# Optimization experiments

Hardware: AMD Instinct MI355X
Metric: run time of the kernel (lower is better)

Reference implementation:

```python
import jax, jax.numpy as jnp
import numpy as np

T, B, E, H, V = 50, 64, 1024, 1024, 32000
NL = 2


def setup_inputs() -> dict:
    key = jax.random.key(0)
    ks = jax.random.split(key, 16)
    def rn(k, shape, fan_in):
        return jax.random.normal(k, shape, jnp.float32) * (1.0 / np.sqrt(fan_in))
    return {
        "word": jax.random.randint(ks[0], (B,), 0, V),
        "seq": jax.random.randint(ks[1], (T, B), 0, V),
        "emb": jax.random.normal(ks[2], (V, E), jnp.float32) * 0.05,
        "w2h_W": rn(ks[3], (H, E), E),
        "w2h_b": jnp.zeros((H,), jnp.float32),
        "W_ih0": rn(ks[4], (4 * H, 2 * E), 2 * E),
        "W_hh0": rn(ks[5], (4 * H, H), H),
        "b_ih0": jnp.zeros((4 * H,), jnp.float32),
        "b_hh0": jnp.zeros((4 * H,), jnp.float32),
        "W_ih1": rn(ks[6], (4 * H, H), H),
        "W_hh1": rn(ks[7], (4 * H, H), H),
        "b_ih1": jnp.zeros((4 * H,), jnp.float32),
        "b_hh1": jnp.zeros((4 * H,), jnp.float32),
        "dec_W": rn(ks[8], (V, H), H),
        "dec_b": jnp.zeros((V,), jnp.float32),
    }


def _lstm_layer(x, Wih, Whh, bih, bhh, h0, c0):
    """x: [T,B,D] -> hs: [T,B,H]. PyTorch gate order: i,f,g,o."""
    b = bih + bhh
    # precompute input contribution for all timesteps (one big GEMM)
    xg = jnp.einsum('tbd,gd->tbg', x, Wih) + b  # [T,B,4H]

    def step(carry, xt):
        h, c = carry
        gates = xt + h @ Whh.T
        i, f, g, o = jnp.split(gates, 4, axis=-1)
        c = jax.nn.sigmoid(f) * c + jax.nn.sigmoid(i) * jnp.tanh(g)
        h = jax.nn.sigmoid(o) * jnp.tanh(c)
        return (h, c), h

    (hT, cT), hs = jax.lax.scan(step, (h0, c0), xg)
    return hs, hT, cT


def reference(word, seq, emb, w2h_W, w2h_b, W_ih0, W_hh0, b_ih0, b_hh0,
              W_ih1, W_hh1, b_ih1, b_hh1, dec_W, dec_b):
    word_emb = emb[word]            # [B,E]
    seq_emb = emb[seq]              # [T,B,E]
    # init_hidden: c = word2hidden(word_emb) expanded over layers, h = zeros
    c0 = word_emb @ w2h_W.T + w2h_b          # [B,H]
    h0 = jnp.zeros_like(c0)
    # use_input: concat word_emb to every timestep input
    x0 = jnp.concatenate(
        [jnp.broadcast_to(word_emb[None], (T, B, E)), seq_emb], axis=-1)  # [T,B,2E]
    hs0, h0T, c0T = _lstm_layer(x0, W_ih0, W_hh0, b_ih0, b_hh0, h0, c0)
    hs1, h1T, c1T = _lstm_layer(hs0, W_ih1, W_hh1, b_ih1, b_hh1, h0, c0)
    outputs = hs1.reshape(T * B, H)
    decoded = outputs @ dec_W.T + dec_b      # [T*B, V]
    h_final = jnp.stack([h0T, h1T], 0)       # [NL,B,H]
    c_final = jnp.stack([c0T, c1T], 0)
    return decoded, h_final, c_final
```

## Files before the change

### kernel.cpp

```cpp
#include <hip/hip_runtime.h>
#include <cstddef>


static constexpr int T_ = 50, B_ = 64, E_ = 1024, H_ = 1024, V_ = 32000;
static constexpr int G_ = 4096;

typedef unsigned short u16;
typedef unsigned int u32;
typedef unsigned long long u64;
typedef __attribute__((ext_vector_type(8))) short bf16x8;
typedef __attribute__((ext_vector_type(8))) unsigned short u16x8;
typedef __attribute__((ext_vector_type(4))) float f32x4;

__device__ __forceinline__ int perm_g(int n) {
  return ((n >> 4) & 3) * H_ + (n >> 6) * 16 + (n & 15);
}
__device__ __forceinline__ u16 bf16_rn(float x) {
  union { float f; unsigned u; } a; a.f = x;
  unsigned r = a.u + 0x7fffu + ((a.u >> 16) & 1u);
  return (u16)(r >> 16);
}
__device__ __forceinline__ float bf16_f(u16 h) {
  union { float f; unsigned u; } a; a.u = ((unsigned)h) << 16;
  return a.f;
}
__device__ __forceinline__ float sigm(float x) { return 1.f / (1.f + __expf(-x)); }

__global__ void fill_zero(float* p, int n) {
  int i = blockIdx.x * blockDim.x + threadIdx.x;
  if (i < n) p[i] = 0.f;
}
__global__ void bias_perm(const float* a, const float* b, float* dst) {
  int n = blockIdx.x * 256 + threadIdx.x;
  int s = perm_g(n);
  dst[n] = a[s] + b[s];
}

__global__ void conv_w(const float* __restrict__ src, int srcld, int coloff,
                       const int* __restrict__ gidx, int PERM, int rows,
                       u16* __restrict__ dst) {
  int idx = blockIdx.x * 256 + threadIdx.x;
  int r = idx >> 7, kc = (idx & 127) << 3;
  if (r >= rows) return;
  int s = gidx ? gidx[r] : (PERM ? perm_g(r) : r);
  const float* p = src + (size_t)s * srcld + coloff + kc;
  float4 v0 = *(const float4*)p, v1 = *(const float4*)(p + 4);
  float vv[8] = {v0.x, v0.y, v0.z, v0.w, v1.x, v1.y, v1.z, v1.w};
  u16 hi[8], lo[8];
#pragma unroll
  for (int i = 0; i < 8; ++i) {
    hi[i] = bf16_rn(vv[i]);
    lo[i] = bf16_rn(vv[i] - bf16_f(hi[i]));
  }
  u16x8 c0, c1;
#pragma unroll
  for (int i = 0; i < 4; ++i) {
    c0[2 * i] = hi[i];     c0[2 * i + 1] = lo[i];
    c1[2 * i] = hi[4 + i]; c1[2 * i + 1] = lo[4 + i];
  }
  int seg = kc >> 5;
  int ch0 = (kc >> 2) & 7;
  size_t base = (size_t)r * 2048 + seg * 64;
  *(u16x8*)&dst[base + (size_t)((ch0 ^ (r & 7)) << 3)] = c0;
  *(u16x8*)&dst[base + (size_t)(((ch0 | 1) ^ (r & 7)) << 3)] = c1;
}

template<int BM, int BN, int BK, int TM, int TN>
__launch_bounds__(256)
__global__ void gemm_nt(
    const float* __restrict__ A, const int* __restrict__ Aidx, int lda,
    const float* __restrict__ W, int ldw, int koff,
    const float* __restrict__ bias, float* __restrict__ C, int ldc,
    int M, int N, int K) {
  constexpr int TX = BN / TN;
  constexpr int TY = BM / TM;
  static_assert(TX * TY == 256, "thread geometry");
  __shared__ float As[BK][BM + 4];
  __shared__ float Ws[BK][BN + 4];
  const int tid = threadIdx.x;
  const int tx = tid % TX, ty = tid / TX;
  const int m0 = blockIdx.y * BM, n0 = blockIdx.x * BN;
  float acc[TM][TN];
#pragma unroll
  for (int i = 0; i < TM; ++i)
#pragma unroll
    for (int j = 0; j < TN; ++j) acc[i][j] = 0.f;
  constexpr int AV = (BM * BK) / 4;
  constexpr int WV = (BN * BK) / 4;
  constexpr int KV = BK / 4;
  for (int k0 = 0; k0 < K; k0 += BK) {
#pragma unroll
    for (int lp = 0; lp < (AV + 255) / 256; ++lp) {
      int e = tid + lp * 256;
      if (e < AV) {
        int r = e / KV, kq = e % KV;
        int m = m0 + r;
        float4 v = make_float4(0.f, 0.f, 0.f, 0.f);
        if (m < M) {
          int row = Aidx ? Aidx[m] : m;
          v = *(const float4*)&A[(size_t)row * lda + k0 + kq * 4];
        }
        As[kq * 4 + 0][r] = v.x; As[kq * 4 + 1][r] = v.y;
        As[kq * 4 + 2][r] = v.z; As[kq * 4 + 3][r] = v.w;
      }
    }
#pragma unroll
    for (int lp = 0; lp < (WV + 255) / 256; ++lp) {
      int e = tid + lp * 256;
      if (e < WV) {
        int cc = e / KV, kq = e % KV;
        int n = n0 + cc;
        float4 v = make_float4(0.f, 0.f, 0.f, 0.f);
        if (n < N)
          v = *(const float4*)&W[(size_t)n * ldw + koff + k0 + kq * 4];
        Ws[kq * 4 + 0][cc] = v.x; Ws[kq * 4 + 1][cc] = v.y;
        Ws[kq * 4 + 2][cc] = v.z; Ws[kq * 4 + 3][cc] = v.w;
      }
    }
    __syncthreads();
#pragma unroll
    for (int kk = 0; kk < BK; ++kk) {
      float a[TM], b[TN];
#pragma unroll
      for (int i = 0; i < TM; ++i) a[i] = As[kk][ty * TM + i];
#pragma unroll
      for (int j = 0; j < TN; ++j) b[j] = Ws[kk][tx * TN + j];
#pragma unroll
      for (int i = 0; i < TM; ++i)
#pragma unroll
        for (int j = 0; j < TN; ++j)
          acc[i][j] += a[i] * b[j];
    }
    __syncthreads();
  }
#pragma unroll
  for (int i = 0; i < TM; ++i) {
    int m = m0 + ty * TM + i;
    if (m >= M) continue;
#pragma unroll
    for (int j = 0; j < TN; ++j) {
      int n = n0 + tx * TN + j;
      if (n >= N) continue;
      float v = acc[i][j];
      if (bias) v += bias[n];
      C[(size_t)m * ldc + n] = v;
    }
  }
}

__launch_bounds__(256)
__global__ void gemm_bt(const u16* __restrict__ A, int Mrows,
                        const u16* __restrict__ Wb,
                        const float* __restrict__ bias,
                        const float* __restrict__ Dadd, int ldd, int dmask,
                        float* __restrict__ C, int ldc, int N, int nbx,
                        int mt, int ord) {
  __shared__ u16 lsA[128 * 64];
  __shared__ u16 lsB[128 * 64];

  int nwg = gridDim.x, bid = blockIdx.x;
  int q = nwg >> 3, r = nwg & 7;
  int xcd = bid & 7, base = bid >> 3;
  int wg = (xcd < r ? xcd * (q + 1) : r * (q + 1) + (xcd - r) * q) + base;
  int bx, by;
  if (ord) { by = wg % mt; bx = wg / mt; } else { bx = wg % nbx; by = wg / nbx; }
  const int m0 = by * 128, n0 = bx * 128;

  const int tid = threadIdx.x, w = tid >> 6, l = tid & 63;
  const int lr = l & 15, lq = l >> 4;
  const int wm = (w >> 1) * 64, wn = (w & 1) * 64;

  f32x4 acc[4][4] = {};

  for (int kt = 0; kt < 32; ++kt) {
#pragma unroll
    for (int i = 0; i < 4; ++i) {
      int rb = w * 32 + i * 8;
      int gm = m0 + rb + (l >> 3);
      if (gm > Mrows - 1) gm = Mrows - 1;
      const u16* ga = A + (size_t)gm * 2048 + kt * 64 + (l & 7) * 8;
      __builtin_amdgcn_global_load_lds(
          (const __attribute__((address_space(1))) void*)ga,
          (__attribute__((address_space(3))) void*)(lsA + rb * 64), 16, 0, 0);
      const u16* gb = Wb + (size_t)(n0 + rb + (l >> 3)) * 2048 + kt * 64 + (l & 7) * 8;
      __builtin_amdgcn_global_load_lds(
          (const __attribute__((address_space(1))) void*)gb,
          (__attribute__((address_space(3))) void*)(lsB + rb * 64), 16, 0, 0);
    }
    asm volatile("s_waitcnt vmcnt(0)" ::: "memory");
    __syncthreads();

    bf16x8 af[4][2], bfr[4][2];
#pragma unroll
    for (int i = 0; i < 4; ++i) {
      int ar = wm + i * 16 + lr;
#pragma unroll
      for (int s = 0; s < 2; ++s)
        af[i][s] = *(const bf16x8*)&lsA[ar * 64 + (((s << 2) + lq) ^ (ar & 7)) * 8];
    }
#pragma unroll
    for (int j = 0; j < 4; ++j) {
      int br = wn + j * 16 + lr;
#pragma unroll
      for (int s = 0; s < 2; ++s)
        bfr[j][s] = *(const bf16x8*)&lsB[br * 64 + (((s << 2) + lq) ^ (br & 7)) * 8];
    }
#pragma unroll
    for (int i = 0; i < 4; ++i)
#pragma unroll
      for (int j = 0; j < 4; ++j) {
        acc[i][j] = __builtin_amdgcn_mfma_f32_16x16x32_bf16(af[i][0], bfr[j][0], acc[i][j], 0, 0, 0);
        acc[i][j] = __builtin_amdgcn_mfma_f32_16x16x32_bf16(af[i][1], bfr[j][1], acc[i][j], 0, 0, 0);
      }
    __syncthreads();
  }

#pragma unroll
  for (int i = 0; i < 4; ++i) {
    int mbase = m0 + wm + i * 16 + lq * 4;
#pragma unroll
    for (int j = 0; j < 4; ++j) {
      int n = n0 + wn + j * 16 + lr;
      float badd = bias ? bias[n] : 0.f;
#pragma unroll
      for (int rr = 0; rr < 4; ++rr) {
        int m = mbase + rr;
        if (m >= Mrows) continue;
        float v = acc[i][j][rr] + badd;
        if (Dadd) {
          int dr = (dmask < 0) ? m : (m & dmask);
          v += Dadd[(size_t)dr * ldd + n];
        }
        C[(size_t)m * ldc + n] = v;
      }
    }
  }
}

__launch_bounds__(256)
__global__ void gemm_sp(
    const float* __restrict__ A, int lda,
    const float* __restrict__ W, int ldw,
    const float* __restrict__ bias,
    float* __restrict__ C, int ldc, int M, int N, int K, int nbx) {
  __shared__ u16 As_h[128][40], As_l[128][40];
  __shared__ u16 Ws_h[128][40], Ws_l[128][40];
  int nwg = gridDim.x, bid = blockIdx.x;
  int q = nwg >> 3, r = nwg & 7;
  int xcd = bid & 7, base = bid >> 3;
  int wg = (xcd < r ? xcd * (q + 1) : r * (q + 1) + (xcd - r) * q) + base;
  int bx = wg % nbx, by = wg / nbx;
  const int m0 = by * 128, n0 = bx * 128;
  const int tid = threadIdx.x;
  const int wave = tid >> 6, lane = tid & 63;
  const int lr = lane & 15, lq = lane >> 4;
  const int wm = (wave >> 1) * 64, wn = (wave & 1) * 64;
  f32x4 acc[4][4] = {};
  for (int k0 = 0; k0 < K; k0 += 32) {
#pragma unroll
    for (int lp = 0; lp < 4; ++lp) {
      int s = tid + lp * 256;
      int row = s >> 3, kq = s & 7;
      float4 v = make_float4(0.f, 0.f, 0.f, 0.f);
      int gm = m0 + row;
      if (gm < M)
        v = *(const float4*)&A[(size_t)gm * lda + k0 + kq * 4];
      u16 h0 = bf16_rn(v.x), h1 = bf16_rn(v.y), h2 = bf16_rn(v.z), h3 = bf16_rn(v.w);
      u16 l0 = bf16_rn(v.x - bf16_f(h0)), l1 = bf16_rn(v.y - bf16_f(h1));
      u16 l2 = bf16_rn(v.z - bf16_f(h2)), l3 = bf16_rn(v.w - bf16_f(h3));
      *(uint2*)&As_h[row][kq * 4] =
          make_uint2((u32)h0 | ((u32)h1 << 16), (u32)h2 | ((u32)h3 << 16));
      *(uint2*)&As_l[row][kq * 4] =
          make_uint2((u32)l0 | ((u32)l1 << 16), (u32)l2 | ((u32)l3 << 16));
    }
#pragma unroll
    for (int lp = 0; lp < 4; ++lp) {
      int s = tid + lp * 256;
      int col = s >> 3, kq = s & 7;
      int n = n0 + col;
      float4 v = make_float4(0.f, 0.f, 0.f, 0.f);
      if (n < N)
        v = *(const float4*)&W[(size_t)n * ldw + k0 + kq * 4];
      u16 h0 = bf16_rn(v.x), h1 = bf16_rn(v.y), h2 = bf16_rn(v.z), h3 = bf16_rn(v.w);
      u16 l0 = bf16_rn(v.x - bf16_f(h0)), l1 = bf16_rn(v.y - bf16_f(h1));
      u16 l2 = bf16_rn(v.z - bf16_f(h2)), l3 = bf16_rn(v.w - bf16_f(h3));
      *(uint2*)&Ws_h[col][kq * 4] =
          make_uint2((u32)h0 | ((u32)h1 << 16), (u32)h2 | ((u32)h3 << 16));
      *(uint2*)&Ws_l[col][kq * 4] =
          make_uint2((u32)l0 | ((u32)l1 << 16), (u32)l2 | ((u32)l3 << 16));
    }
    __syncthreads();
    bf16x8 ah[4], al[4], bh[4], bl[4];
#pragma unroll
    for (int i = 0; i < 4; ++i) {
      ah[i] = *(const bf16x8*)&As_h[wm + i * 16 + lr][lq * 8];
      al[i] = *(const bf16x8*)&As_l[wm + i * 16 + lr][lq * 8];
    }
#pragma unroll
    for (int j = 0; j < 4; ++j) {
      bh[j] = *(const bf16x8*)&Ws_h[wn + j * 16 + lr][lq * 8];
      bl[j] = *(const bf16x8*)&Ws_l[wn + j * 16 + lr][lq * 8];
    }
#pragma unroll
    for (int i = 0; i < 4; ++i)
#pragma unroll
      for (int j = 0; j < 4; ++j) {
        acc[i][j] = __builtin_amdgcn_mfma_f32_16x16x32_bf16(ah[i], bh[j], acc[i][j], 0, 0, 0);
        acc[i][j] = __builtin_amdgcn_mfma_f32_16x16x32_bf16(ah[i], bl[j], acc[i][j], 0, 0, 0);
        acc[i][j] = __builtin_amdgcn_mfma_f32_16x16x32_bf16(al[i], bh[j], acc[i][j], 0, 0, 0);
      }
    __syncthreads();
  }
#pragma unroll
  for (int i = 0; i < 4; ++i) {
    int mbase = m0 + wm + i * 16 + lq * 4;
#pragma unroll
    for (int j = 0; j < 4; ++j) {
      int n = n0 + wn + j * 16 + lr;
      if (n >= N) continue;
      float badd = bias ? bias[n] : 0.f;
#pragma unroll
      for (int rr = 0; rr < 4; ++rr) {
        int m = mbase + rr;
        if (m >= M) continue;
        C[(size_t)m * ldc + n] = acc[i][j][rr] + badd;
      }
    }
  }
}

__device__ __forceinline__ void gemm_half(
    const u32* __restrict__ hp, int rg, int w, int lr, int lq,
    const bf16x8 (&bfr)[8][4], f32x4 (&acc)[2][4]) {
  bf16x8 af[8][2];
#pragma unroll
  for (int s = 0; s < 8; ++s)
#pragma unroll
    for (int mt = 0; mt < 2; ++mt) {
      int m = rg * 32 + mt * 16 + lr;
      int seg = w * 4 + (s >> 1);
      int cis = ((((s & 1) << 2) + lq) ^ (lr & 7));
      const u32* p = hp + (size_t)m * 1024 + seg * 32 + cis * 4;
      asm volatile("global_load_dwordx4 %0, %1, off sc0 sc1"
                   : "=v"(af[s][mt]) : "v"(p) : "memory");
    }
  asm volatile("s_waitcnt vmcnt(0)" ::: "memory");
  __builtin_amdgcn_sched_barrier(0);
#pragma unroll
  for (int s = 0; s < 8; ++s)
#pragma unroll
    for (int mt = 0; mt < 2; ++mt)
#pragma unroll
      for (int nt = 0; nt < 4; ++nt)
        acc[mt][nt] = __builtin_amdgcn_mfma_f32_16x16x32_bf16(
            af[s][mt], bfr[s][nt], acc[mt][nt], 0, 0, 0);
}

__device__ __forceinline__ void poll_flags(const u32* flags, int rg, int l, u32 tgt) {
  int guard = 0;
  for (;;) {
    u32 v = __hip_atomic_load(flags + (size_t)((rg << 6) + l) * 4,
                              __ATOMIC_RELAXED, __HIP_MEMORY_SCOPE_AGENT);
    if (__all(v >= tgt)) break;
    if (++guard > (1 << 23)) break;
    __builtin_amdgcn_s_sleep(1);
  }
}

template<bool DUAL, bool EMIT>
__launch_bounds__(512, 1)
__global__ void rnn_dual(const u16* __restrict__ Whh0b, const u16* __restrict__ Whh1b,
                         const u16* __restrict__ Wih1b,
                         const float* __restrict__ xg0all, const float* __restrict__ bias1p,
                         float* __restrict__ cL0, float* __restrict__ hL0,
                         float* __restrict__ cL1, float* __restrict__ hL1,
                         u32* __restrict__ h0s, u32* __restrict__ h1s,
                         float* __restrict__ hsf,
                         u32* __restrict__ flg0, u32* __restrict__ flg1, int T) {
  __shared__ float partial[8][32][68];

  const int bid = blockIdx.x;
  const int x = bid & 7, j = bid >> 3;
  const int layer = DUAL ? (j & 1) : 0;
  const int idx = DUAL ? (j >> 1) : j;
  const int ct = x * 8 + (idx & 7);
  const int rg = idx >> 3;
  const int tid = threadIdx.x, w = tid >> 6, l = tid & 63;
  const int lr = l & 15, lq = l >> 4;

  const u16* WbA = (layer ? Whh1b : Whh0b) + (size_t)(ct * 64) * 2048;
  bf16x8 bfragA[8][4];
#pragma unroll
  for (int s = 0; s < 8; ++s)
#pragma unroll
    for (int nt = 0; nt < 4; ++nt) {
      int row = nt * 16 + lr;
      int seg = w * 4 + (s >> 1);
      int cis = ((((s & 1) << 2) + lq) ^ (lr & 7));
      bfragA[s][nt] = *(const bf16x8*)&WbA[(size_t)row * 2048 + seg * 64 + cis * 8];
    }
  bf16x8 bfragX[8][4];
  if (DUAL && layer) {
    const u16* WbX = Wih1b + (size_t)(ct * 64) * 2048;
#pragma unroll
    for (int s = 0; s < 8; ++s)
#pragma unroll
      for (int nt = 0; nt < 4; ++nt) {
        int row = nt * 16 + lr;
        int seg = w * 4 + (s >> 1);
        int cis = ((((s & 1) << 2) + lq) ^ (lr & 7));
        bfragX[s][nt] = *(const bf16x8*)&WbX[(size_t)row * 2048 + seg * 64 + cis * 8];
      }
  }

  const int cm = tid >> 4, cu = tid & 15;
  const int m_c = rg * 32 + cm;
  const int unit = ct * 16 + cu;
  float* cL = layer ? cL1 : cL0;
  float* hL = layer ? hL1 : hL0;
  u32* hsl = layer ? h1s : h0s;
  u32* flgS = layer ? flg1 : flg0;
  float creg = cL[m_c * H_ + unit];
  float bset[4];
  if (layer) {
#pragma unroll
    for (int g = 0; g < 4; ++g)
      bset[g] = bias1p[ct * 64 + g * 16 + cu];
  }

  for (int t = 0; t < T; ++t) {
    float xgv[4];
    if (!layer) {
      const float* xg = xg0all + (size_t)t * ((size_t)B_ * G_);
#pragma unroll
      for (int g = 0; g < 4; ++g)
        xgv[g] = xg[(size_t)m_c * G_ + ct * 64 + g * 16 + cu];
    } else {
#pragma unroll
      for (int g = 0; g < 4; ++g) xgv[g] = bset[g];
    }

    f32x4 acc[2][4] = {};

    if (layer) {
      if (t && w == 0) poll_flags(flg1, rg, l, (u32)t);
      __syncthreads();
      gemm_half(h1s + (size_t)t * (B_ * 1024), rg, w, lr, lq, bfragA, acc);
      if (w == 0) poll_flags(flg0, rg, l, (u32)(t + 1));
      __syncthreads();
      gemm_half(h0s + (size_t)(t + 1) * (B_ * 1024), rg, w, lr, lq, bfragX, acc);
    } else {
      if (t && w == 0) poll_flags(flg0, rg, l, (u32)t);
      __syncthreads();
      gemm_half(h0s + (size_t)t * (B_ * 1024), rg, w, lr, lq, bfragA, acc);
    }

#pragma unroll
    for (int mt = 0; mt < 2; ++mt)
#pragma unroll
      for (int nt = 0; nt < 4; ++nt)
#pragma unroll
        for (int rr = 0; rr < 4; ++rr)
          partial[w][mt * 16 + lq * 4 + rr][nt * 16 + lr] = acc[mt][nt][rr];
    __syncthreads();

    float g4[4];
#pragma unroll
    for (int g = 0; g < 4; ++g) {
      float ssum = xgv[g];
#pragma unroll
      for (int p = 0; p < 8; ++p) ssum += partial[p][cm][g * 16 + cu];
      g4[g] = ssum;
    }
    float cn = sigm(g4[1]) * creg + sigm(g4[0]) * tanhf(g4[2]);
    float hn = sigm(g4[3]) * tanhf(cn);
    creg = cn;
    if (EMIT && layer) hsf[(size_t)t * (B_ * H_) + m_c * H_ + unit] = hn;
    if (t == T - 1) { cL[m_c * H_ + unit] = cn; hL[m_c * H_ + unit] = hn; }
    u16 hh = bf16_rn(hn);
    u16 hl2 = bf16_rn(hn - bf16_f(hh));
    u32 packed = (u32)hh | ((u32)hl2 << 16);
    u32* hnext = hsl + (size_t)(t + 1) * (B_ * 1024);
    u32 hidx = m_c * 1024 + ((unit >> 5) << 5) +
               ((((unit >> 2) & 7) ^ (m_c & 7)) << 2) + (unit & 3);
    {
      u32* sp = hnext + hidx;
      asm volatile("global_store_dword %0, %1, off sc0 sc1"
                   :: "v"(sp), "v"(packed) : "memory");
    }

    if (!layer || t < T - 1) {
      asm volatile("s_waitcnt vmcnt(0)" ::: "memory");
      __syncthreads();
      if (tid == 0)
        __hip_atomic_store(flgS + (size_t)((rg << 6) + ct) * 4, (u32)(t + 1),
                           __ATOMIC_RELAXED, __HIP_MEMORY_SCOPE_AGENT);
    }
  }
}

__launch_bounds__(256)
__global__ void rnn_step(const u16* __restrict__ hprev, const u16* __restrict__ Wb,
                         const float* __restrict__ xg,
                         float* __restrict__ c, float* __restrict__ hf,
                         u32* __restrict__ hout) {
  __shared__ char smem[32768];
  u16* lsA = (u16*)smem;
  u16* lsB = (u16*)(smem + 16384);
  const int nt = blockIdx.x, n0 = nt * 64;
  const int tid = threadIdx.x, w = tid >> 6, l = tid & 63;
  const int lr = l & 15, lq = l >> 4;
  f32x4 acc[4] = {};
  for (int kt = 0; kt < 16; ++kt) {
#pragma unroll
    for (int i = 0; i < 4; ++i) {
      int rb = w * 16 + i * 4;
      const u16* ga = hprev + (size_t)(rb + (l >> 4)) * 2048 + kt * 128 + (l & 15) * 8;
      __builtin_amdgcn_global_load_lds(
          (const __attribute__((address_space(1))) void*)ga,
          (__attribute__((address_space(3))) void*)(lsA + rb * 128), 16, 0, 0);
      const u16* gb = Wb + (size_t)(n0 + rb + (l >> 4)) * 2048 + kt * 128 + (l & 15) * 8;
      __builtin_amdgcn_global_load_lds(
          (const __attribute__((address_space(1))) void*)gb,
          (__attribute__((address_space(3))) void*)(lsB + rb * 128), 16, 0, 0);
    }
    asm volatile("s_waitcnt vmcnt(0)" ::: "memory");
    __syncthreads();
    bf16x8 af[4];
    int ar = w * 16 + lr;
#pragma unroll
    for (int s = 0; s < 4; ++s)
      af[s] = *(const bf16x8*)&lsA[ar * 128 + (s >> 1) * 64 + ((((s & 1) << 2) + lq) ^ (ar & 7)) * 8];
#pragma unroll
    for (int j = 0; j < 4; ++j) {
      int br = j * 16 + lr;
#pragma unroll
      for (int s = 0; s < 4; ++s) {
        bf16x8 bv = *(const bf16x8*)&lsB[br * 128 + (s >> 1) * 64 + ((((s & 1) << 2) + lq) ^ (br & 7)) * 8];
        acc[j] = __builtin_amdgcn_mfma_f32_16x16x32_bf16(af[s], bv, acc[j], 0, 0, 0);
      }
    }
    __syncthreads();
  }
  float* gsh = (float*)smem;
#pragma unroll
  for (int j = 0; j < 4; ++j)
#pragma unroll
    for (int rr = 0; rr < 4; ++rr)
      gsh[(w * 16 + lq * 4 + rr) * 68 + j * 16 + lr] = acc[j][rr];
  __syncthreads();
  const int ui = tid & 15, mq = tid >> 4;
#pragma unroll
  for (int mr = 0; mr < 4; ++mr) {
    int m = mr * 16 + mq;
    float gi = gsh[m * 68 + 0 + ui]  + xg[(size_t)m * G_ + n0 + 0 + ui];
    float gf = gsh[m * 68 + 16 + ui] + xg[(size_t)m * G_ + n0 + 16 + ui];
    float gg = gsh[m * 68 + 32 + ui] + xg[(size_t)m * G_ + n0 + 32 + ui];
    float go = gsh[m * 68 + 48 + ui] + xg[(size_t)m * G_ + n0 + 48 + ui];
    int unit = nt * 16 + ui;
    int ci = m * H_ + unit;
    float cn = sigm(gf) * c[ci] + sigm(gi) * tanhf(gg);
    float hn = sigm(go) * tanhf(cn);
    c[ci] = cn;
    hf[ci] = hn;
    u16 hh = bf16_rn(hn);
    u16 hl = bf16_rn(hn - bf16_f(hh));
    u32 hidx = m * 1024 + ((unit >> 5) << 5) +
               ((((unit >> 2) & 7) ^ (m & 7)) << 2) + (unit & 3);
    hout[hidx] = (u32)hh | ((u32)hl << 16);
  }
}

extern "C" void kernel_launch(void* const* d_in, const int* in_sizes, int n_in,
                              void* d_out, int out_size, void* d_ws, size_t ws_size,
                              hipStream_t stream) {
  const int*   word  = (const int*)  d_in[0];
  const int*   seq   = (const int*)  d_in[1];
  const float* emb   = (const float*)d_in[2];
  const float* w2h_W = (const float*)d_in[3];
  const float* w2h_b = (const float*)d_in[4];
  const float* W_ih0 = (const float*)d_in[5];
  const float* W_hh0 = (const float*)d_in[6];
  const float* b_ih0 = (const float*)d_in[7];
  const float* b_hh0 = (const float*)d_in[8];
  const float* W_ih1 = (const float*)d_in[9];
  const float* W_hh1 = (const float*)d_in[10];
  const float* b_ih1 = (const float*)d_in[11];
  const float* b_hh1 = (const float*)d_in[12];
  const float* dec_W = (const float*)d_in[13];
  const float* dec_b = (const float*)d_in[14];

  float* out = (float*)d_out;
  float* hL0 = out + 102400000;
  float* hL1 = hL0 + B_ * H_;
  float* cL0 = out + 102531072;
  float* cL1 = cL0 + B_ * H_;

  float* xg0      = out;
  u16*   x0w_bf   = (u16*)(out + 13200000);
  u16*   x0seq_bf = (u16*)(out + 13300000);
  u32*   hs0slots = (u32*)(out + 16600000);
  u16*   wih0a_bf = (u16*)(out + 20000000);
  u16*   wih0b_bf = (u16*)(out + 24200000);
  u16*   wih1_bf  = (u16*)(out + 28400000);
  u16*   whh0_bf  = (u16*)(out + 32600000);
  u16*   whh1_bf  = (u16*)(out + 36800000);
  float* y_w      = out + 73800000;
  float* bias0p   = out + 74400000;
  float* bias1p   = out + 74410000;
  float* xg1      = out + 87560192;
  u32*   h1alt    = (u32*)(out + 91000000);
  u32*   flg0     = (u32*)(out + 101000000);
  u32*   flg1     = (u32*)(out + 101004096);
  u32*   hbfA     = (u32*)(out + 101100000);
  u32*   hbfB     = (u32*)(out + 101200000);

  const size_t need_hs1  = (size_t)T_ * B_ * H_ * 4;
  const size_t need_full = (size_t)V_ * 2048 * 2 + (size_t)(T_ + 1) * B_ * 1024 * 4;
  const bool tier1 = ws_size >= need_full;
  const bool tier2 = !tier1 && ws_size >= need_hs1;

  u16*   decW_bf  = (u16*)d_ws;
  u32*   hs1slots = (u32*)d_ws + (size_t)V_ * 1024;
  float* hs1f     = (float*)d_ws;

  fill_zero<<<32, 256, 0, stream>>>(out + 101000000, 8192);
  fill_zero<<<256, 256, 0, stream>>>((float*)hs0slots, 65536);
  if (tier1) fill_zero<<<256, 256, 0, stream>>>((float*)hs1slots, 65536);
  else if (tier2) fill_zero<<<256, 256, 0, stream>>>((float*)h1alt, 65536);
  bias_perm<<<16, 256, 0, stream>>>(b_ih0, b_hh0, bias0p);
  bias_perm<<<16, 256, 0, stream>>>(b_ih1, b_hh1, bias1p);

  gemm_nt<64, 64, 16, 4, 4><<<dim3(16, 1), 256, 0, stream>>>(
      emb, word, E_, w2h_W, E_, 0, w2h_b, cL0, H_, B_, H_, E_);
  gemm_nt<64, 64, 16, 4, 4><<<dim3(16, 1), 256, 0, stream>>>(
      emb, word, E_, w2h_W, E_, 0, w2h_b, cL1, H_, B_, H_, E_);

  conv_w<<<2048, 256, 0, stream>>>(W_ih0, 2 * E_, 0,  nullptr, 1, G_, wih0a_bf);
  conv_w<<<2048, 256, 0, stream>>>(W_ih0, 2 * E_, E_, nullptr, 1, G_, wih0b_bf);
  conv_w<<<2048, 256, 0, stream>>>(W_ih1, H_, 0, nullptr, 1, G_, wih1_bf);
  conv_w<<<2048, 256, 0, stream>>>(W_hh0, H_, 0, nullptr, 1, G_, whh0_bf);
  conv_w<<<2048, 256, 0, stream>>>(W_hh1, H_, 0, nullptr, 1, G_, whh1_bf);
  conv_w<<<32,   256, 0, stream>>>(emb, E_, 0, word, 0, B_, x0w_bf);
  conv_w<<<1600, 256, 0, stream>>>(emb, E_, 0, seq, 0, T_ * B_, x0seq_bf);
  if (tier1)
    conv_w<<<16000, 256, 0, stream>>>(dec_W, H_, 0, nullptr, 0, V_, decW_bf);

  gemm_bt<<<32, 256, 0, stream>>>(x0w_bf, B_, wih0a_bf, bias0p,
                                  nullptr, 0, -1, y_w, G_, G_, 32, 1, 0);
  gemm_bt<<<800, 256, 0, stream>>>(x0seq_bf, T_ * B_, wih0b_bf, nullptr,
                                   y_w, G_, 63, xg0, G_, G_, 32, 25, 0);

  if (tier1) {
    rnn_dual<true, false><<<256, 512, 0, stream>>>(
        whh0_bf, whh1_bf, wih1_bf, xg0, bias1p,
        cL0, hL0, cL1, hL1, hs0slots, hs1slots, nullptr, flg0, flg1, T_);
    gemm_bt<<<6250, 256, 0, stream>>>((const u16*)(hs1slots + (size_t)B_ * 1024),
                                      T_ * B_, decW_bf, dec_b,
                                      nullptr, 0, -1, out, V_, V_, 250, 25, 1);
  } else if (tier2) {
    rnn_dual<true, true><<<256, 512, 0, stream>>>(
        whh0_bf, whh1_bf, wih1_bf, xg0, bias1p,
        cL0, hL0, cL1, hL1, hs0slots, h1alt, hs1f, flg0, flg1, T_);
    gemm_sp<<<6250, 256, 0, stream>>>(
        hs1f, H_, dec_W, H_, dec_b, out, V_, T_ * B_, V_, H_, 250);
  } else {
    rnn_dual<false, false><<<128, 512, 0, stream>>>(
        whh0_bf, whh1_bf, wih1_bf, xg0, bias1p,
        cL0, hL0, cL1, hL1, hs0slots, nullptr, nullptr, flg0, flg1, T_);
    gemm_bt<<<800, 256, 0, stream>>>((const u16*)(hs0slots + (size_t)B_ * 1024),
                                     T_ * B_, wih1_bf, bias1p,
                                     nullptr, 0, -1, xg1, G_, G_, 32, 25, 0);
    for (int t = 0; t < T_; ++t) {
      const u16* hp = t ? (const u16*)((t & 1) ? hbfA : hbfB) : (const u16*)hs0slots;
      u32* ho = (t & 1) ? hbfB : hbfA;
      rnn_step<<<64, 256, 0, stream>>>(
          hp, whh1_bf, xg1 + (size_t)t * B_ * G_, cL1, hL1, ho);
      gemm_sp<<<250, 256, 0, stream>>>(
          hL1, H_, dec_W, H_, dec_b, out + (size_t)t * B_ * V_, V_, B_, V_, H_, 250);
    }
  }
}
```

Measured before the change: 1.851 ms.

## Fuse decoder GEMM into persistent LSTM kernel, overlapping chunks with recurrence

Adds a decode_chunk routine inside the persistent rnn_dual kernel. Every 4 timesteps, each of the first 250 blocks waits on the layer-1 flags and computes 256 rows of the vocab projection. It converts fp32 dec_W to split bf16 hi/lo on the fly instead of running a separate conversion pass and a trailing decoder GEMM. A new workspace tier holds h states, xg0 and the converted recurrent weights. The aim is to hide the large decoder GEMM behind the latency-bound recurrence, at the cost of extra LDS (96KB), extra barriers that may stall the recurrence critical path, and repeated dec_W conversion per chunk.

Result: slower. 2.520 ms (+36.2%).

```diff
diff --git a/kernel.cpp b/kernel.cpp
--- a/kernel.cpp
+++ b/kernel.cpp
@@ -367,7 +367,88 @@
   }
 }
 
-template<bool DUAL, bool EMIT>
+__device__ __forceinline__ void decode_chunk(
+    char* smem, int ch, int nMt, int n0,
+    const u32* __restrict__ h1s, const float* __restrict__ decW,
+    const float* __restrict__ dec_b, float* __restrict__ outC,
+    int tid, int w, int lr, int lq) {
+  u16* As = (u16*)smem;
+  u16* Bs = (u16*)(smem + 65536);
+  const int nrows = nMt * 64;
+  f32x4 acc[4][4] = {};
+
+  for (int kc = 0; kc < 16; ++kc) {
+    __syncthreads();
+#pragma unroll
+    for (int i = 0; i < 8; ++i) {
+      int e = tid + i * 512;
+      int row = e >> 4, part = e & 15;
+      if (row < nrows) {
+        const u32* src = h1s + (size_t)(4 * ch + 1 + (row >> 6)) * (B_ * 1024)
+                       + (size_t)(row & 63) * 1024 + kc * 64 + part * 4;
+        uint4 v = *(const uint4*)src;
+        *(uint4*)&As[row * 128 + part * 8] = v;
+      }
+    }
+#pragma unroll
+    for (int i = 0; i < 2; ++i) {
+      int e = tid + i * 512;
+      int row = e >> 3, kc8 = e & 7;
+      const float* p = decW + (size_t)(n0 + row) * 1024 + kc * 64 + kc8 * 8;
+      float4 v0 = *(const float4*)p, v1 = *(const float4*)(p + 4);
+      float vv[8] = {v0.x, v0.y, v0.z, v0.w, v1.x, v1.y, v1.z, v1.w};
+      u16 hi[8], lo[8];
+#pragma unroll
+      for (int q2 = 0; q2 < 8; ++q2) {
+        hi[q2] = bf16_rn(vv[q2]);
+        lo[q2] = bf16_rn(vv[q2] - bf16_f(hi[q2]));
+      }
+      u16x8 c0, c1;
+#pragma unroll
+      for (int q2 = 0; q2 < 4; ++q2) {
+        c0[2 * q2] = hi[q2];     c0[2 * q2 + 1] = lo[q2];
+        c1[2 * q2] = hi[4 + q2]; c1[2 * q2 + 1] = lo[4 + q2];
+      }
+      int segl = kc8 >> 2;
+      int ch0 = (kc8 & 3) * 2;
+      u16* dst = Bs + row * 128 + segl * 64;
+      *(u16x8*)&dst[(ch0 ^ (row & 7)) << 3] = c0;
+      *(u16x8*)&dst[((ch0 | 1) ^ (row & 7)) << 3] = c1;
+    }
+    __syncthreads();
+#pragma unroll
+    for (int ks = 0; ks < 4; ++ks) {
+      int segl = ks >> 1;
+      int cgrp = (ks & 1) << 2;
+      int cis = (cgrp + lq) ^ (lr & 7);
+      bf16x8 bfr = *(const bf16x8*)&Bs[(w * 16 + lr) * 128 + segl * 64 + cis * 8];
+#pragma unroll
+      for (int mt = 0; mt < 4; ++mt)
+#pragma unroll
+        for (int mf = 0; mf < 4; ++mf) {
+          int row = mt * 64 + mf * 16 + lr;
+          bf16x8 af = *(const bf16x8*)&As[row * 128 + segl * 64 + cis * 8];
+          acc[mt][mf] = __builtin_amdgcn_mfma_f32_16x16x32_bf16(af, bfr, acc[mt][mf], 0, 0, 0);
+        }
+    }
+  }
+  __syncthreads();
+  int col = n0 + w * 16 + lr;
+  float badd = dec_b[col];
+#pragma unroll
+  for (int mt = 0; mt < 4; ++mt) {
+    if (mt >= nMt) break;
+#pragma unroll
+    for (int mf = 0; mf < 4; ++mf)
+#pragma unroll
+      for (int rr = 0; rr < 4; ++rr) {
+        int mrow = ch * 256 + mt * 64 + mf * 16 + lq * 4 + rr;
+        outC[(size_t)mrow * V_ + col] = acc[mt][mf][rr] + badd;
+      }
+  }
+}
+
+template<bool DUAL, bool EMIT, bool DEC>
 __launch_bounds__(512, 1)
 __global__ void rnn_dual(const u16* __restrict__ Whh0b, const u16* __restrict__ Whh1b,
                          const u16* __restrict__ Wih1b,
@@ -376,8 +457,11 @@
                          float* __restrict__ cL1, float* __restrict__ hL1,
                          u32* __restrict__ h0s, u32* __restrict__ h1s,
                          float* __restrict__ hsf,
-                         u32* __restrict__ flg0, u32* __restrict__ flg1, int T) {
-  __shared__ float partial[8][32][68];
+                         u32* __restrict__ flg0, u32* __restrict__ flg1,
+                         const float* __restrict__ decW, const float* __restrict__ dec_b,
+                         float* __restrict__ outC, int T) {
+  __shared__ char smem[98304];
+  float* partial = (float*)smem;
 
   const int bid = blockIdx.x;
   const int x = bid & 7, j = bid >> 3;
@@ -461,7 +545,7 @@
       for (int nt = 0; nt < 4; ++nt)
 #pragma unroll
         for (int rr = 0; rr < 4; ++rr)
-          partial[w][mt * 16 + lq * 4 + rr][nt * 16 + lr] = acc[mt][nt][rr];
+          partial[(w * 32 + mt * 16 + lq * 4 + rr) * 68 + nt * 16 + lr] = acc[mt][nt][rr];
     __syncthreads();
 
     float g4[4];
@@ -469,7 +553,7 @@
     for (int g = 0; g < 4; ++g) {
       float ssum = xgv[g];
 #pragma unroll
-      for (int p = 0; p < 8; ++p) ssum += partial[p][cm][g * 16 + cu];
+      for (int p = 0; p < 8; ++p) ssum += partial[(p * 32 + cm) * 68 + g * 16 + cu];
       g4[g] = ssum;
     }
     float cn = sigm(g4[1]) * creg + sigm(g4[0]) * tanhf(g4[2]);
@@ -489,13 +573,30 @@
                    :: "v"(sp), "v"(packed) : "memory");
     }
 
-    if (!layer || t < T - 1) {
-      asm volatile("s_waitcnt vmcnt(0)" ::: "memory");
-      __syncthreads();
-      if (tid == 0)
-        __hip_atomic_store(flgS + (size_t)((rg << 6) + ct) * 4, (u32)(t + 1),
-                           __ATOMIC_RELAXED, __HIP_MEMORY_SCOPE_AGENT);
-    }
+    asm volatile("s_waitcnt vmcnt(0)" ::: "memory");
+    __syncthreads();
+    if (tid == 0)
+      __hip_atomic_store(flgS + (size_t)((rg << 6) + ct) * 4, (u32)(t + 1),
+                         __ATOMIC_RELAXED, __HIP_MEMORY_SCOPE_AGENT);
+
+    if (DEC) {
+      if (t >= 5 && ((t - 5) & 3) == 0) {
+        int ch = (t - 5) >> 2;
+        u32 tgt = (u32)(4 * ch + 4);
+        if (w == 0) { poll_flags(flg1, 0, l, tgt); poll_flags(flg1, 1, l, tgt); }
+        __syncthreads();
+        if (bid < 250)
+          decode_chunk(smem, ch, 4, bid * 128, h1s, decW, dec_b, outC, tid, w, lr, lq);
+        __syncthreads();
+      }
+    }
+  }
+
+  if (DEC) {
+    if (w == 0) { poll_flags(flg1, 0, l, (u32)T); poll_flags(flg1, 1, l, (u32)T); }
+    __syncthreads();
+    if (bid < 250)
+      decode_chunk(smem, 12, 2, bid * 128, h1s, decW, dec_b, outC, tid, w, lr, lq);
   }
 }
 
@@ -532,22 +633,22 @@
     for (int s = 0; s < 4; ++s)
       af[s] = *(const bf16x8*)&lsA[ar * 128 + (s >> 1) * 64 + ((((s & 1) << 2) + lq) ^ (ar & 7)) * 8];
 #pragma unroll
-    for (int j = 0; j < 4; ++j) {
-      int br = j * 16 + lr;
+    for (int jj = 0; jj < 4; ++jj) {
+      int br = jj * 16 + lr;
 #pragma unroll
       for (int s = 0; s < 4; ++s) {
         bf16x8 bv = *(const bf16x8*)&lsB[br * 128 + (s >> 1) * 64 + ((((s & 1) << 2) + lq) ^ (br & 7)) * 8];
-        acc[j] = __builtin_amdgcn_mfma_f32_16x16x32_bf16(af[s], bv, acc[j], 0, 0, 0);
+        acc[jj] = __builtin_amdgcn_mfma_f32_16x16x32_bf16(af[s], bv, acc[jj], 0, 0, 0);
       }
     }
     __syncthreads();
   }
   float* gsh = (float*)smem;
 #pragma unroll
-  for (int j = 0; j < 4; ++j)
+  for (int jj = 0; jj < 4; ++jj)
 #pragma unroll
     for (int rr = 0; rr < 4; ++rr)
-      gsh[(w * 16 + lq * 4 + rr) * 68 + j * 16 + lr] = acc[j][rr];
+      gsh[(w * 16 + lq * 4 + rr) * 68 + jj * 16 + lr] = acc[jj][rr];
   __syncthreads();
   const int ui = tid & 15, mq = tid >> 4;
 #pragma unroll
@@ -596,88 +697,120 @@
   float* cL0 = out + 102531072;
   float* cL1 = cL0 + B_ * H_;
 
-  float* xg0      = out;
   u16*   x0w_bf   = (u16*)(out + 13200000);
   u16*   x0seq_bf = (u16*)(out + 13300000);
-  u32*   hs0slots = (u32*)(out + 16600000);
   u16*   wih0a_bf = (u16*)(out + 20000000);
   u16*   wih0b_bf = (u16*)(out + 24200000);
-  u16*   wih1_bf  = (u16*)(out + 28400000);
-  u16*   whh0_bf  = (u16*)(out + 32600000);
-  u16*   whh1_bf  = (u16*)(out + 36800000);
   float* y_w      = out + 73800000;
   float* bias0p   = out + 74400000;
-  float* bias1p   = out + 74410000;
-  float* xg1      = out + 87560192;
-  u32*   h1alt    = (u32*)(out + 91000000);
-  u32*   flg0     = (u32*)(out + 101000000);
-  u32*   flg1     = (u32*)(out + 101004096);
-  u32*   hbfA     = (u32*)(out + 101100000);
-  u32*   hbfB     = (u32*)(out + 101200000);
-
-  const size_t need_hs1  = (size_t)T_ * B_ * H_ * 4;
-  const size_t need_full = (size_t)V_ * 2048 * 2 + (size_t)(T_ + 1) * B_ * 1024 * 4;
-  const bool tier1 = ws_size >= need_full;
-  const bool tier2 = !tier1 && ws_size >= need_hs1;
-
-  u16*   decW_bf  = (u16*)d_ws;
-  u32*   hs1slots = (u32*)d_ws + (size_t)V_ * 1024;
-  float* hs1f     = (float*)d_ws;
-
-  fill_zero<<<32, 256, 0, stream>>>(out + 101000000, 8192);
-  fill_zero<<<256, 256, 0, stream>>>((float*)hs0slots, 65536);
-  if (tier1) fill_zero<<<256, 256, 0, stream>>>((float*)hs1slots, 65536);
-  else if (tier2) fill_zero<<<256, 256, 0, stream>>>((float*)h1alt, 65536);
-  bias_perm<<<16, 256, 0, stream>>>(b_ih0, b_hh0, bias0p);
-  bias_perm<<<16, 256, 0, stream>>>(b_ih1, b_hh1, bias1p);
-
-  gemm_nt<64, 64, 16, 4, 4><<<dim3(16, 1), 256, 0, stream>>>(
-      emb, word, E_, w2h_W, E_, 0, w2h_b, cL0, H_, B_, H_, E_);
-  gemm_nt<64, 64, 16, 4, 4><<<dim3(16, 1), 256, 0, stream>>>(
-      emb, word, E_, w2h_W, E_, 0, w2h_b, cL1, H_, B_, H_, E_);
-
-  conv_w<<<2048, 256, 0, stream>>>(W_ih0, 2 * E_, 0,  nullptr, 1, G_, wih0a_bf);
-  conv_w<<<2048, 256, 0, stream>>>(W_ih0, 2 * E_, E_, nullptr, 1, G_, wih0b_bf);
-  conv_w<<<2048, 256, 0, stream>>>(W_ih1, H_, 0, nullptr, 1, G_, wih1_bf);
-  conv_w<<<2048, 256, 0, stream>>>(W_hh0, H_, 0, nullptr, 1, G_, whh0_bf);
-  conv_w<<<2048, 256, 0, stream>>>(W_hh1, H_, 0, nullptr, 1, G_, whh1_bf);
-  conv_w<<<32,   256, 0, stream>>>(emb, E_, 0, word, 0, B_, x0w_bf);
-  conv_w<<<1600, 256, 0, stream>>>(emb, E_, 0, seq, 0, T_ * B_, x0seq_bf);
-  if (tier1)
-    conv_w<<<16000, 256, 0, stream>>>(dec_W, H_, 0, nullptr, 0, V_, decW_bf);
-
-  gemm_bt<<<32, 256, 0, stream>>>(x0w_bf, B_, wih0a_bf, bias0p,
-                                  nullptr, 0, -1, y_w, G_, G_, 32, 1, 0);
-  gemm_bt<<<800, 256, 0, stream>>>(x0seq_bf, T_ * B_, wih0b_bf, nullptr,
-                                   y_w, G_, 63, xg0, G_, G_, 32, 25, 0);
-
-  if (tier1) {
-    rnn_dual<true, false><<<256, 512, 0, stream>>>(
-        whh0_bf, whh1_bf, wih1_bf, xg0, bias1p,
-        cL0, hL0, cL1, hL1, hs0slots, hs1slots, nullptr, flg0, flg1, T_);
-    gemm_bt<<<6250, 256, 0, stream>>>((const u16*)(hs1slots + (size_t)B_ * 1024),
-                                      T_ * B_, decW_bf, dec_b,
-                                      nullptr, 0, -1, out, V_, V_, 250, 25, 1);
-  } else if (tier2) {
-    rnn_dual<true, true><<<256, 512, 0, stream>>>(
-        whh0_bf, whh1_bf, wih1_bf, xg0, bias1p,
-        cL0, hL0, cL1, hL1, hs0slots, h1alt, hs1f, flg0, flg1, T_);
-    gemm_sp<<<6250, 256, 0, stream>>>(
-        hs1f, H_, dec_W, H_, dec_b, out, V_, T_ * B_, V_, H_, 250);
+
+  const size_t need0    = 129600000;
+  const size_t need_hs1 = (size_t)T_ * B_ * H_ * 4;
+  const bool tier0 = ws_size >= need0;
+  const bool tier2 = !tier0 && ws_size >= need_hs1;
+
+  if (tier0) {
+    char* wsb = (char*)d_ws;
+    u32*   h1p    = (u32*)wsb;
+    u32*   h0p    = (u32*)(wsb + 13369344);
+    float* xg0p   = (float*)(wsb + 26738688);
+    u16*   whh0p  = (u16*)(wsb + 79167488);
+    u16*   whh1p  = (u16*)(wsb + 95944704);
+    u16*   wih1p  = (u16*)(wsb + 112721920);
+    float* b1p    = (float*)(wsb + 129499136);
+    u32*   f0p    = (u32*)(wsb + 129515520);
+    u32*   f1p    = (u32*)(wsb + 129519616);
+
+    fill_zero<<<8, 256, 0, stream>>>((float*)f0p, 2048);
+    fill_zero<<<256, 256, 0, stream>>>((float*)h0p, 65536);
+    fill_zero<<<256, 256, 0, stream>>>((float*)h1p, 65536);
+    bias_perm<<<16, 256, 0, stream>>>(b_ih0, b_hh0, bias0p);
+    bias_perm<<<16, 256, 0, stream>>>(b_ih1, b_hh1, b1p);
+
+    gemm_nt<64, 64, 16, 4, 4><<<dim3(16, 1), 256, 0, stream>>>(
+        emb, word, E_, w2h_W, E_, 0, w2h_b, cL0, H_, B_, H_, E_);
+    gemm_nt<64, 64, 16, 4, 4><<<dim3(16, 1), 256, 0, stream>>>(
+        emb, word, E_, w2h_W, E_, 0, w2h_b, cL1, H_, B_, H_, E_);
+
+    conv_w<<<2048, 256, 0, stream>>>(W_ih0, 2 * E_, 0,  nullptr, 1, G_, wih0a_bf);
+    conv_w<<<2048, 256, 0, stream>>>(W_ih0, 2 * E_, E_, nullptr, 1, G_, wih0b_bf);
+    conv_w<<<2048, 256, 0, stream>>>(W_ih1, H_, 0, nullptr, 1, G_, wih1p);
+    conv_w<<<2048, 256, 0, stream>>>(W_hh0, H_, 0, nullptr, 1, G_, whh0p);
+    conv_w<<<2048, 256, 0, stream>>>(W_hh1, H_, 0, nullptr, 1, G_, whh1p);
+    conv_w<<<32,   256, 0, stream>>>(emb, E_, 0, word, 0, B_, x0w_bf);
+    conv_w<<<1600, 256, 0, stream>>>(emb, E_, 0, seq, 0, T_ * B_, x0seq_bf);
+
+    gemm_bt<<<32, 256, 0, stream>>>(x0w_bf, B_, wih0a_bf, bias0p,
+                                    nullptr, 0, -1, y_w, G_, G_, 32, 1, 0);
+    gemm_bt<<<800, 256, 0, stream>>>(x0seq_bf, T_ * B_, wih0b_bf, nullptr,
+                                     y_w, G_, 63, xg0p, G_, G_, 32, 25, 0);
+
+    rnn_dual<true, false, true><<<256, 512, 0, stream>>>(
+        whh0p, whh1p, wih1p, xg0p, b1p,
+        cL0, hL0, cL1, hL1, h0p, h1p, nullptr, f0p, f1p,
+        dec_W, dec_b, out, T_);
   } else {
-    rnn_dual<false, false><<<128, 512, 0, stream>>>(
-        whh0_bf, whh1_bf, wih1_bf, xg0, bias1p,
-        cL0, hL0, cL1, hL1, hs0slots, nullptr, nullptr, flg0, flg1, T_);
-    gemm_bt<<<800, 256, 0, stream>>>((const u16*)(hs0slots + (size_t)B_ * 1024),
-                                     T_ * B_, wih1_bf, bias1p,
-                                     nullptr, 0, -1, xg1, G_, G_, 32, 25, 0);
-    for (int t = 0; t < T_; ++t) {
-      const u16* hp = t ? (const u16*)((t & 1) ? hbfA : hbfB) : (const u16*)hs0slots;
-      u32* ho = (t & 1) ? hbfB : hbfA;
-      rnn_step<<<64, 256, 0, stream>>>(
-          hp, whh1_bf, xg1 + (size_t)t * B_ * G_, cL1, hL1, ho);
-      gemm_sp<<<250, 256, 0, stream>>>(
-          hL1, H_, dec_W, H_, dec_b, out + (size_t)t * B_ * V_, V_, B_, V_, H_, 250);
-    }
-  }
-}
+    float* xg0      = out;
+    u32*   hs0slots = (u32*)(out + 16600000);
+    u16*   wih1_bf  = (u16*)(out + 28400000);
+    u16*   whh0_bf  = (u16*)(out + 32600000);
+    u16*   whh1_bf  = (u16*)(out + 36800000);
+    float* bias1p   = out + 74410000;
+    float* xg1      = out + 87560192;
+    u32*   h1alt    = (u32*)(out + 91000000);
+    u32*   flg0     = (u32*)(out + 101000000);
+    u32*   flg1     = (u32*)(out + 101004096);
+    u32*   hbfA     = (u32*)(out + 101100000);
+    u32*   hbfB     = (u32*)(out + 101200000);
+    float* hs1f     = (float*)d_ws;
+
+    fill_zero<<<32, 256, 0, stream>>>(out + 101000000, 8192);
+    fill_zero<<<256, 256, 0, stream>>>((float*)hs0slots, 65536);
+    if (tier2) fill_zero<<<256, 256, 0, stream>>>((float*)h1alt, 65536);
+    bias_perm<<<16, 256, 0, stream>>>(b_ih0, b_hh0, bias0p);
+    bias_perm<<<16, 256, 0, stream>>>(b_ih1, b_hh1, bias1p);
+
+    gemm_nt<64, 64, 16, 4, 4><<<dim3(16, 1), 256, 0, stream>>>(
+        emb, word, E_, w2h_W, E_, 0, w2h_b, cL0, H_, B_, H_, E_);
+    gemm_nt<64, 64, 16, 4, 4><<<dim3(16, 1), 256, 0, stream>>>(
+        emb, word, E_, w2h_W, E_, 0, w2h_b, cL1, H_, B_, H_, E_);
+
+    conv_w<<<2048, 256, 0, stream>>>(W_ih0, 2 * E_, 0,  nullptr, 1, G_, wih0a_bf);
+    conv_w<<<2048, 256, 0, stream>>>(W_ih0, 2 * E_, E_, nullptr, 1, G_, wih0b_bf);
+    conv_w<<<2048, 256, 0, stream>>>(W_ih1, H_, 0, nullptr, 1, G_, wih1_bf);
+    conv_w<<<2048, 256, 0, stream>>>(W_hh0, H_, 0, nullptr, 1, G_, whh0_bf);
+    conv_w<<<2048, 256, 0, stream>>>(W_hh1, H_, 0, nullptr, 1, G_, whh1_bf);
+    conv_w<<<32,   256, 0, stream>>>(emb, E_, 0, word, 0, B_, x0w_bf);
+    conv_w<<<1600, 256, 0, stream>>>(emb, E_, 0, seq, 0, T_ * B_, x0seq_bf);
+
+    gemm_bt<<<32, 256, 0, stream>>>(x0w_bf, B_, wih0a_bf, bias0p,
+                                    nullptr, 0, -1, y_w, G_, G_, 32, 1, 0);
+    gemm_bt<<<800, 256, 0, stream>>>(x0seq_bf, T_ * B_, wih0b_bf, nullptr,
+                                     y_w, G_, 63, xg0, G_, G_, 32, 25, 0);
+
+    if (tier2) {
+      rnn_dual<true, true, false><<<256, 512, 0, stream>>>(
+          whh0_bf, whh1_bf, wih1_bf, xg0, bias1p,
+          cL0, hL0, cL1, hL1, hs0slots, h1alt, hs1f, flg0, flg1,
+          nullptr, nullptr, nullptr, T_);
+      gemm_sp<<<6250, 256, 0, stream>>>(
+          hs1f, H_, dec_W, H_, dec_b, out, V_, T_ * B_, V_, H_, 250);
+    } else {
+      rnn_dual<false, false, false><<<128, 512, 0, stream>>>(
+          whh0_bf, whh1_bf, wih1_bf, xg0, bias1p,
+          cL0, hL0, cL1, hL1, hs0slots, nullptr, nullptr, flg0, flg1,
+          nullptr, nullptr, nullptr, T_);
+      gemm_bt<<<800, 256, 0, stream>>>((const u16*)(hs0slots + (size_t)B_ * 1024),
+                                       T_ * B_, wih1_bf, bias1p,
+                                       nullptr, 0, -1, xg1, G_, G_, 32, 25, 0);
+      for (int t = 0; t < T_; ++t) {
+        const u16* hp = t ? (const u16*)((t & 1) ? hbfA : hbfB) : (const u16*)hs0slots;
+        u32* ho = (t & 1) ? hbfB : hbfA;
+        rnn_step<<<64, 256, 0, stream>>>(
+            hp, whh1_bf, xg1 + (size_t)t * B_ * G_, cL1, hL1, ho);
+        gemm_sp<<<250, 256, 0, stream>>>(
+            hL1, H_, dec_W, H_, dec_b, out + (size_t)t * B_ * V_, V_, B_, V_, H_, 250);
+      }
+    }
+  }
+}
```

## Double-buffer gemm_bt LDS loads and let each wave poll its own source flags

Applied to the files above, without the earlier changes.

The main bf16 GEMM now uses two LDS buffers and issues the global-to-LDS loads for the next k-tile before computing on the current one. It waits with a partial vmcnt so memory latency overlaps the MFMA work. In the recurrent kernel, each wave now polls only the 8 producer flags it depends on, replacing one wave polling all flags followed by a block-wide barrier. This removes a __syncthreads per GEMM half, at the cost of doubled LDS use in gemm_bt and a finer-grained dependency check that must cover every row each wave reads.

After: 2.006 ms. 1.08x slower.

```diff
diff --git a/kernel.cpp b/kernel.cpp
--- a/kernel.cpp
+++ b/kernel.cpp
@@ -155,8 +155,8 @@
                         const float* __restrict__ Dadd, int ldd, int dmask,
                         float* __restrict__ C, int ldc, int N, int nbx,
                         int mt, int ord) {
-  __shared__ u16 lsA[128 * 64];
-  __shared__ u16 lsB[128 * 64];
+  __shared__ u16 lsA[2][128 * 64];
+  __shared__ u16 lsB[2][128 * 64];
 
   int nwg = gridDim.x, bid = blockIdx.x;
   int q = nwg >> 3, r = nwg & 7;
@@ -172,22 +172,33 @@
 
   f32x4 acc[4][4] = {};
 
+#define GBT_STAGE(KT, BUF)                                                     \
+  {                                                                            \
+    _Pragma("unroll")                                                          \
+    for (int i_ = 0; i_ < 4; ++i_) {                                           \
+      int rb_ = w * 32 + i_ * 8;                                               \
+      int gm_ = m0 + rb_ + (l >> 3);                                           \
+      if (gm_ > Mrows - 1) gm_ = Mrows - 1;                                    \
+      const u16* ga_ = A + (size_t)gm_ * 2048 + (KT) * 64 + (l & 7) * 8;       \
+      __builtin_amdgcn_global_load_lds(                                        \
+          (const __attribute__((address_space(1))) void*)ga_,                  \
+          (__attribute__((address_space(3))) void*)(lsA[BUF] + rb_ * 64), 16, 0, 0); \
+      const u16* gb_ = Wb + (size_t)(n0 + rb_ + (l >> 3)) * 2048 + (KT) * 64 + (l & 7) * 8; \
+      __builtin_amdgcn_global_load_lds(                                        \
+          (const __attribute__((address_space(1))) void*)gb_,                  \
+          (__attribute__((address_space(3))) void*)(lsB[BUF] + rb_ * 64), 16, 0, 0); \
+    }                                                                          \
+  }
+
+  GBT_STAGE(0, 0)
   for (int kt = 0; kt < 32; ++kt) {
-#pragma unroll
-    for (int i = 0; i < 4; ++i) {
-      int rb = w * 32 + i * 8;
-      int gm = m0 + rb + (l >> 3);
-      if (gm > Mrows - 1) gm = Mrows - 1;
-      const u16* ga = A + (size_t)gm * 2048 + kt * 64 + (l & 7) * 8;
-      __builtin_amdgcn_global_load_lds(
-          (const __attribute__((address_space(1))) void*)ga,
-          (__attribute__((address_space(3))) void*)(lsA + rb * 64), 16, 0, 0);
-      const u16* gb = Wb + (size_t)(n0 + rb + (l >> 3)) * 2048 + kt * 64 + (l & 7) * 8;
-      __builtin_amdgcn_global_load_lds(
-          (const __attribute__((address_space(1))) void*)gb,
-          (__attribute__((address_space(3))) void*)(lsB + rb * 64), 16, 0, 0);
-    }
-    asm volatile("s_waitcnt vmcnt(0)" ::: "memory");
+    const int cur = kt & 1;
+    if (kt < 31) {
+      GBT_STAGE(kt + 1, cur ^ 1)
+      asm volatile("s_waitcnt vmcnt(8)" ::: "memory");
+    } else {
+      asm volatile("s_waitcnt vmcnt(0)" ::: "memory");
+    }
     __syncthreads();
 
     bf16x8 af[4][2], bfr[4][2];
@@ -196,14 +207,14 @@
       int ar = wm + i * 16 + lr;
 #pragma unroll
       for (int s = 0; s < 2; ++s)
-        af[i][s] = *(const bf16x8*)&lsA[ar * 64 + (((s << 2) + lq) ^ (ar & 7)) * 8];
+        af[i][s] = *(const bf16x8*)&lsA[cur][ar * 64 + (((s << 2) + lq) ^ (ar & 7)) * 8];
     }
 #pragma unroll
     for (int j = 0; j < 4; ++j) {
       int br = wn + j * 16 + lr;
 #pragma unroll
       for (int s = 0; s < 2; ++s)
-        bfr[j][s] = *(const bf16x8*)&lsB[br * 64 + (((s << 2) + lq) ^ (br & 7)) * 8];
+        bfr[j][s] = *(const bf16x8*)&lsB[cur][br * 64 + (((s << 2) + lq) ^ (br & 7)) * 8];
     }
 #pragma unroll
     for (int i = 0; i < 4; ++i)
@@ -214,6 +225,7 @@
       }
     __syncthreads();
   }
+#undef GBT_STAGE
 
 #pragma unroll
   for (int i = 0; i < 4; ++i) {
@@ -356,11 +368,13 @@
             af[s][mt], bfr[s][nt], acc[mt][nt], 0, 0, 0);
 }
 
-__device__ __forceinline__ void poll_flags(const u32* flags, int rg, int l, u32 tgt) {
+__device__ __forceinline__ void poll_src(const u32* flags, int rg, int w, int l, u32 tgt) {
   int guard = 0;
   for (;;) {
-    u32 v = __hip_atomic_load(flags + (size_t)((rg << 6) + l) * 4,
-                              __ATOMIC_RELAXED, __HIP_MEMORY_SCOPE_AGENT);
+    u32 v = tgt;
+    if (l < 8)
+      v = __hip_atomic_load(flags + (size_t)((rg << 6) + (w << 3) + l) * 4,
+                            __ATOMIC_RELAXED, __HIP_MEMORY_SCOPE_AGENT);
     if (__all(v >= tgt)) break;
     if (++guard > (1 << 23)) break;
     __builtin_amdgcn_s_sleep(1);
@@ -443,15 +457,12 @@
     f32x4 acc[2][4] = {};
 
     if (layer) {
-      if (t && w == 0) poll_flags(flg1, rg, l, (u32)t);
-      __syncthreads();
+      if (t) poll_src(flg1, rg, w, l, (u32)t);
       gemm_half(h1s + (size_t)t * (B_ * 1024), rg, w, lr, lq, bfragA, acc);
-      if (w == 0) poll_flags(flg0, rg, l, (u32)(t + 1));
-      __syncthreads();
+      poll_src(flg0, rg, w, l, (u32)(t + 1));
       gemm_half(h0s + (size_t)(t + 1) * (B_ * 1024), rg, w, lr, lq, bfragX, acc);
     } else {
-      if (t && w == 0) poll_flags(flg0, rg, l, (u32)t);
-      __syncthreads();
+      if (t) poll_src(flg0, rg, w, l, (u32)t);
       gemm_half(h0s + (size_t)t * (B_ * 1024), rg, w, lr, lq, bfragA, acc);
     }
 
@@ -532,22 +543,22 @@
     for (int s = 0; s < 4; ++s)
       af[s] = *(const bf16x8*)&lsA[ar * 128 + (s >> 1) * 64 + ((((s & 1) << 2) + lq) ^ (ar & 7)) * 8];
 #pragma unroll
-    for (int j = 0; j < 4; ++j) {
-      int br = j * 16 + lr;
+    for (int jj = 0; jj < 4; ++jj) {
+      int br = jj * 16 + lr;
 #pragma unroll
       for (int s = 0; s < 4; ++s) {
         bf16x8 bv = *(const bf16x8*)&lsB[br * 128 + (s >> 1) * 64 + ((((s & 1) << 2) + lq) ^ (br & 7)) * 8];
-        acc[j] = __builtin_amdgcn_mfma_f32_16x16x32_bf16(af[s], bv, acc[j], 0, 0, 0);
+        acc[jj] = __builtin_amdgcn_mfma_f32_16x16x32_bf16(af[s], bv, acc[jj], 0, 0, 0);
       }
     }
     __syncthreads();
   }
   float* gsh = (float*)smem;
 #pragma unroll
-  for (int j = 0; j < 4; ++j)
+  for (int jj = 0; jj < 4; ++jj)
 #pragma unroll
     for (int rr = 0; rr < 4; ++rr)
-      gsh[(w * 16 + lq * 4 + rr) * 68 + j * 16 + lr] = acc[j][rr];
+      gsh[(w * 16 + lq * 4 + rr) * 68 + jj * 16 + lr] = acc[jj][rr];
   __syncthreads();
   const int ui = tid & 15, mq = tid >> 4;
 #pragma unroll
```
